# Performance work log

Hardware: AMD Instinct MI355X
Metric: run time of the kernel (lower is better)

The kernel has to match this reference:

```python
import jax, jax.numpy as jnp
import numpy as np

N = 500000   # nodes per batched graph
D = 64       # per-graph node feature dim (encoded_dims // 2)
P = 1000000  # number of interface candidate pairs
ED = 2 * D   # encoded_dims = 128


def setup_inputs() -> dict:
    key = jax.random.key(0)
    k1, k2, k3, k4, k5, k6 = jax.random.split(key, 6)
    graph1_x = jax.random.normal(k1, (N, D), dtype=jnp.float32)
    graph2_x = jax.random.normal(k2, (N, D), dtype=jnp.float32)
    idx_left = jax.random.randint(k3, (P,), 0, N, dtype=jnp.int32).astype(jnp.int64)
    idx_right = jax.random.randint(k4, (P,), 0, N, dtype=jnp.int32).astype(jnp.int64)
    W1 = jax.random.normal(k5, (ED, ED), dtype=jnp.float32) * (1.0 / np.sqrt(ED))
    b1 = jnp.zeros((ED,), dtype=jnp.float32)
    W2 = jax.random.normal(k6, (1, ED), dtype=jnp.float32) * (1.0 / np.sqrt(ED))
    b2 = jnp.zeros((1,), dtype=jnp.float32)
    return {"graph1_x": graph1_x, "graph2_x": graph2_x,
            "idx_left": idx_left, "idx_right": idx_right,
            "W1": W1, "b1": b1, "W2": W2, "b2": b2}


def reference(graph1_x, graph2_x, idx_left, idx_right, W1, b1, W2, b2):
    # Gather interface node features from both encoded graphs.
    left = graph1_x[idx_left]    # [P, D]
    right = graph2_x[idx_right]  # [P, D]
    x = jnp.concatenate([left, right], axis=1)  # [P, 2D]
    # top_net: Linear -> ReLU -> Dropout(eval: identity) -> Linear
    h = jax.nn.relu(x @ W1.T + b1)  # [P, ED]
    out = h @ W2.T + b2             # [P, 1]
    return out
```

## Files before the change

kernel.cpp:

```cpp
#include <hip/hip_runtime.h>
#include <hip/hip_bf16.h>


typedef __bf16 bf16x8 __attribute__((ext_vector_type(8)));
typedef float f32x16 __attribute__((ext_vector_type(16)));

__device__ __forceinline__ unsigned f2bf(float f) {
  union { float f; unsigned u; } v;
  v.f = f;
  unsigned u = v.u;
  return (u + 0x7fffu + ((u >> 16) & 1u)) >> 16;
}

__global__ __launch_bounds__(256) void w1_frag_kernel(
    const float* __restrict__ W1, uint4* __restrict__ w1f) {
  int t = blockIdx.x * 256 + threadIdx.x;
  int lane = t & 63;
  int nt = (t >> 6) & 3;
  int ks = t >> 8;
  int n = lane & 31, h = lane >> 5;
  const float4* src =
      (const float4*)(W1 + ((nt * 32 + n) * 128 + ks * 16 + h * 8));
  float4 a = src[0], b = src[1];
  uint4 o;
  o.x = f2bf(a.x) | (f2bf(a.y) << 16);
  o.y = f2bf(a.z) | (f2bf(a.w) << 16);
  o.z = f2bf(b.x) | (f2bf(b.y) << 16);
  o.w = f2bf(b.z) | (f2bf(b.w) << 16);
  w1f[t] = o;
}

#define LDS_STRIDE 136

__global__ __launch_bounds__(256, 4) void pip_main_kernel(
    const float* __restrict__ g1, const float* __restrict__ g2,
    const int* __restrict__ il, const int* __restrict__ ir,
    const bf16x8* __restrict__ w1f,
    const float* __restrict__ b1, const float* __restrict__ w2,
    const float* __restrict__ b2,
    float* __restrict__ out, int P) {
  __shared__ unsigned short A[128 * LDS_STRIDE];

  const int t = threadIdx.x;
  const int lane = t & 63;
  const int w = t >> 6;
  const int pair0 = blockIdx.x * 128;

  const int sub = lane & 15;
  const int g = lane >> 4;
  const int side = g & 1;
  const int pairB = (w * 4 + g) >> 1;
  const float* feat = side ? g2 : g1;
  const int* idxarr = side ? ir : il;

  int idxv[16];
#pragma unroll
  for (int j = 0; j < 16; ++j) {
    int gp = pair0 + j * 8 + pairB;
    int pidx = (gp < P) ? gp : (P - 1);
    idxv[j] = idxarr[pidx];
  }
  float4 v[16];
#pragma unroll
  for (int j = 0; j < 16; ++j)
    v[j] = *(const float4*)(feat + (size_t)idxv[j] * 64 + sub * 4);
  __builtin_amdgcn_sched_barrier(0);
#pragma unroll
  for (int j = 0; j < 16; ++j) {
    unsigned lo = f2bf(v[j].x) | (f2bf(v[j].y) << 16);
    unsigned hi = f2bf(v[j].z) | (f2bf(v[j].w) << 16);
    *(uint2*)(A + (j * 8 + pairB) * LDS_STRIDE + side * 64 + sub * 4) =
        make_uint2(lo, hi);
  }
  __syncthreads();

  const int n = lane & 31;
  const int h = lane >> 5;

  f32x16 acc[4];
#pragma unroll
  for (int nt = 0; nt < 4; ++nt)
#pragma unroll
    for (int i = 0; i < 16; ++i) acc[nt][i] = 0.0f;

  const unsigned short* Arow = A + (w * 32 + n) * LDS_STRIDE + h * 8;
#pragma unroll
  for (int ks = 0; ks < 8; ++ks) {
    bf16x8 af = *(const bf16x8*)(Arow + ks * 16);
#pragma unroll
    for (int nt = 0; nt < 4; ++nt) {
      bf16x8 bfr = w1f[(ks * 4 + nt) * 64 + lane];
      acc[nt] = __builtin_amdgcn_mfma_f32_32x32x16_bf16(af, bfr, acc[nt], 0, 0, 0);
    }
  }

  float b1v[4], w2v[4];
#pragma unroll
  for (int nt = 0; nt < 4; ++nt) {
    b1v[nt] = b1[nt * 32 + n];
    w2v[nt] = w2[nt * 32 + n];
  }
  const float bias2 = b2[0];

#pragma unroll
  for (int r = 0; r < 16; ++r) {
    float s = 0.0f;
#pragma unroll
    for (int nt = 0; nt < 4; ++nt) {
      float vv = acc[nt][r] + b1v[nt];
      vv = fmaxf(vv, 0.0f);
      s = fmaf(vv, w2v[nt], s);
    }
    s += __shfl_xor(s, 1);
    s += __shfl_xor(s, 2);
    s += __shfl_xor(s, 4);
    s += __shfl_xor(s, 8);
    s += __shfl_xor(s, 16);
    if (n == 0) {
      int row = (r & 3) + 8 * (r >> 2) + 4 * h;
      int gp = pair0 + w * 32 + row;
      if (gp < P) out[gp] = s + bias2;
    }
  }
}

extern "C" void kernel_launch(void* const* d_in, const int* in_sizes, int n_in,
                              void* d_out, int out_size, void* d_ws, size_t ws_size,
                              hipStream_t stream) {
  const float* g1 = (const float*)d_in[0];
  const float* g2 = (const float*)d_in[1];
  const int* il = (const int*)d_in[2];
  const int* ir = (const int*)d_in[3];
  const float* W1 = (const float*)d_in[4];
  const float* b1 = (const float*)d_in[5];
  const float* w2 = (const float*)d_in[6];
  const float* b2 = (const float*)d_in[7];
  float* out = (float*)d_out;
  const int P = out_size;

  w1_frag_kernel<<<8, 256, 0, stream>>>(W1, (uint4*)d_ws);

  const int nblocks = (P + 127) / 128;
  pip_main_kernel<<<nblocks, 256, 0, stream>>>(
      g1, g2, il, ir, (const bf16x8*)d_ws, b1, w2, b2, out, P);
}
```

Baseline: 339.0 us.

## Gather features directly into LDS via global_load_lds with XOR swizzle

Replaces the register-staged gather (global load to VGPRs, convert to bf16, store to LDS) with direct global-to-LDS loads that keep fp32 data in an XOR-swizzled layout. The bf16 conversion moves to fragment-load time, using a perm with round-half-up instead of round-to-nearest-even. LDS use doubles to 64KB per block and occupancy drops to 2 blocks per CU, in exchange for fewer VGPRs and no separate conversion and store pass.

```diff
diff --git a/kernel.cpp b/kernel.cpp
--- a/kernel.cpp
+++ b/kernel.cpp
@@ -30,52 +30,52 @@
   w1f[t] = o;
 }
 
-#define LDS_STRIDE 136
-
-__global__ __launch_bounds__(256, 4) void pip_main_kernel(
+__global__ __launch_bounds__(256, 2) void pip_main_kernel(
     const float* __restrict__ g1, const float* __restrict__ g2,
     const int* __restrict__ il, const int* __restrict__ ir,
     const bf16x8* __restrict__ w1f,
     const float* __restrict__ b1, const float* __restrict__ w2,
     const float* __restrict__ b2,
     float* __restrict__ out, int P) {
-  __shared__ unsigned short A[128 * LDS_STRIDE];
+  __shared__ float T[128 * 128];
 
   const int t = threadIdx.x;
   const int lane = t & 63;
   const int w = t >> 6;
   const int pair0 = blockIdx.x * 128;
 
-  const int sub = lane & 15;
+  const int sl = lane & 15;
   const int g = lane >> 4;
   const int side = g & 1;
-  const int pairB = (w * 4 + g) >> 1;
+  const int halfg = lane >> 5;
   const float* feat = side ? g2 : g1;
   const int* idxarr = side ? ir : il;
+  const int plocB = w * 2 + halfg;
 
   int idxv[16];
 #pragma unroll
   for (int j = 0; j < 16; ++j) {
-    int gp = pair0 + j * 8 + pairB;
+    int gp = pair0 + j * 8 + plocB;
     int pidx = (gp < P) ? gp : (P - 1);
     idxv[j] = idxarr[pidx];
   }
-  float4 v[16];
-#pragma unroll
-  for (int j = 0; j < 16; ++j)
-    v[j] = *(const float4*)(feat + (size_t)idxv[j] * 64 + sub * 4);
-  __builtin_amdgcn_sched_barrier(0);
 #pragma unroll
   for (int j = 0; j < 16; ++j) {
-    unsigned lo = f2bf(v[j].x) | (f2bf(v[j].y) << 16);
-    unsigned hi = f2bf(v[j].z) | (f2bf(v[j].w) << 16);
-    *(uint2*)(A + (j * 8 + pairB) * LDS_STRIDE + side * 64 + sub * 4) =
-        make_uint2(lo, hi);
+    int ploc = j * 8 + plocB;
+    const float* src = feat + (size_t)idxv[j] * 64 + ((sl ^ ploc) & 15) * 4;
+    float* dst = &T[(j * 16 + w * 4) * 64];
+    __builtin_amdgcn_global_load_lds(
+        (const __attribute__((address_space(1))) unsigned int*)src,
+        (__attribute__((address_space(3))) unsigned int*)dst, 16, 0, 0);
   }
   __syncthreads();
 
   const int n = lane & 31;
   const int h = lane >> 5;
+  const int p = w * 32 + n;
+  const int key = p & 15;
+  const uint4* As = (const uint4*)T;
+  const int rowbase = p * 32;
 
   f32x16 acc[4];
 #pragma unroll
@@ -83,14 +83,22 @@
 #pragma unroll
     for (int i = 0; i < 16; ++i) acc[nt][i] = 0.0f;
 
-  const unsigned short* Arow = A + (w * 32 + n) * LDS_STRIDE + h * 8;
 #pragma unroll
   for (int ks = 0; ks < 8; ++ks) {
-    bf16x8 af = *(const bf16x8*)(Arow + ks * 16);
+    const int sideK = ks >> 2;
+    const int s0 = (ks & 3) * 4 + h * 2;
+    const int base = rowbase + sideK * 16;
+    uint4 lo = As[base + (s0 ^ key)];
+    uint4 hi = As[base + ((s0 + 1) ^ key)];
+    union { unsigned u[4]; bf16x8 v; } fr;
+    fr.u[0] = __builtin_amdgcn_perm(lo.y + 0x8000u, lo.x + 0x8000u, 0x07060302u);
+    fr.u[1] = __builtin_amdgcn_perm(lo.w + 0x8000u, lo.z + 0x8000u, 0x07060302u);
+    fr.u[2] = __builtin_amdgcn_perm(hi.y + 0x8000u, hi.x + 0x8000u, 0x07060302u);
+    fr.u[3] = __builtin_amdgcn_perm(hi.w + 0x8000u, hi.z + 0x8000u, 0x07060302u);
 #pragma unroll
     for (int nt = 0; nt < 4; ++nt) {
       bf16x8 bfr = w1f[(ks * 4 + nt) * 64 + lane];
-      acc[nt] = __builtin_amdgcn_mfma_f32_32x32x16_bf16(af, bfr, acc[nt], 0, 0, 0);
+      acc[nt] = __builtin_amdgcn_mfma_f32_32x32x16_bf16(fr.v, bfr, acc[nt], 0, 0, 0);
     }
   }
 
```

Result: slower. 373.6 us (+10.2%).
